# Performance work log

Measured on AMD Instinct MI355X. Metric: run time of the kernel, lower is better.

Reference implementation:

```python
import jax, jax.numpy as jnp
import numpy as np

N = 50000          # total nodes across the batched graphs
E = 800000         # edges (before self-loops)
D_IN = 128         # input_dim
D_H = 128          # hidden_channels
N_CLASSES = 2
N_GRAPHS = 64


def setup_inputs() -> dict:
    key = jax.random.key(0)
    ks = jax.random.split(key, 9)
    x = jax.random.normal(ks[0], (N, D_IN), dtype=jnp.float32)
    edge_index = jax.random.randint(ks[1], (2, E), 0, N, dtype=jnp.int64)
    batch = jnp.sort(jax.random.randint(ks[2], (N,), 0, N_GRAPHS, dtype=jnp.int64))
    s1 = 1.0 / np.sqrt(D_IN)
    s2 = 1.0 / np.sqrt(D_H)
    W1 = jax.random.uniform(ks[3], (D_IN, D_H), jnp.float32, -s1, s1)
    b1 = jnp.zeros((D_H,), jnp.float32)
    W2 = jax.random.uniform(ks[4], (D_H, D_H), jnp.float32, -s2, s2)
    b2 = jnp.zeros((D_H,), jnp.float32)
    Wfc = jax.random.uniform(ks[5], (D_H, N_CLASSES), jnp.float32, -s2, s2)
    bfc = jnp.zeros((N_CLASSES,), jnp.float32)
    return {"x": x, "edge_index": edge_index, "batch": batch,
            "W1": W1, "b1": b1, "W2": W2, "b2": b2, "Wfc": Wfc, "bfc": bfc}


def _gcn_conv(x, src, dst, norm, W, b):
    # GCNConv: h = W x, then out_i = sum_{j->i} norm_ij * h_j + b
    h = x @ W                                   # [N, D]
    msg = h[src] * norm[:, None]                # gather + scale, [E+N, D]
    out = jax.ops.segment_sum(msg, dst, num_segments=N)
    return out + b


def reference(x, edge_index, batch, W1, b1, W2, b2, Wfc, bfc):
    loops = jnp.arange(N, dtype=edge_index.dtype)
    src = jnp.concatenate([edge_index[0], loops])  # add self-loops
    dst = jnp.concatenate([edge_index[1], loops])
    # symmetric normalization D^-1/2 (A+I) D^-1/2
    deg = jax.ops.segment_sum(jnp.ones_like(dst, x.dtype), dst, num_segments=N)
    dinv = jax.lax.rsqrt(deg)                      # deg >= 1 due to self-loops
    norm = dinv[src] * dinv[dst]                   # [E+N]

    h = jax.nn.relu(_gcn_conv(x, src, dst, norm, W1, b1))
    h = _gcn_conv(h, src, dst, norm, W2, b2)

    # global_mean_pool over graph ids
    summed = jax.ops.segment_sum(h, batch, num_segments=N_GRAPHS)
    counts = jax.ops.segment_sum(jnp.ones((N,), x.dtype), batch, num_segments=N_GRAPHS)
    pooled = summed / jnp.maximum(counts, 1.0)[:, None]

    return pooled @ Wfc + bfc                      # [N_GRAPHS, N_CLASSES]
```

## Files before the change

### kernel.cpp

```cpp
#include <hip/hip_runtime.h>
#include <hip/hip_fp16.h>


#define N_NODES 50000
#define N_EDGES 800000
#define ETOT (N_EDGES + N_NODES)
#define D 128
#define NG 64
#define NC 2
#define JT 128
#define NBLK_W ((N_NODES + JT - 1) / JT)
#define NODES_PAD (NBLK_W * JT)
#define WT_F4 (NODES_PAD * NG / 4)
#define Q_F4 (NG * D / 4)

__global__ void k_init(int* __restrict__ deg, float4* __restrict__ wT4,
                       float4* __restrict__ q4, float* __restrict__ cnt,
                       int* __restrict__ cursor) {
    int i = blockIdx.x * 256 + threadIdx.x;
    float4 z = {0.f, 0.f, 0.f, 0.f};
    if (i < WT_F4) wT4[i] = z;
    if (i < Q_F4)  q4[i] = z;
    if (i < N_NODES) deg[i] = 1;
    if (i < NG)    cnt[i] = 0.f;
    if (i == 0)    *cursor = 0;
}

__global__ void k_deg(const int* __restrict__ ei, int* __restrict__ deg) {
    int e = blockIdx.x * 256 + threadIdx.x;
    if (e < N_EDGES) atomicAdd(&deg[ei[N_EDGES + e]], 1);
}

__global__ __launch_bounds__(256) void k_off(const int* __restrict__ deg,
                                             int* __restrict__ cursor,
                                             int* __restrict__ off,
                                             int* __restrict__ cur,
                                             float* __restrict__ dinv,
                                             const int* __restrict__ batch,
                                             float* __restrict__ cnt) {
    __shared__ int sh[256];
    __shared__ int base;
    __shared__ float scnt[NG];
    int t = threadIdx.x;
    int n = blockIdx.x * 256 + t;
    if (t < NG) scnt[t] = 0.f;
    int dg = (n < N_NODES) ? deg[n] : 0;
    sh[t] = dg;
    __syncthreads();
    for (int o = 1; o < 256; o <<= 1) {
        int u = (t >= o) ? sh[t - o] : 0;
        __syncthreads();
        sh[t] += u;
        __syncthreads();
    }
    if (t == 255) base = atomicAdd(cursor, sh[255]);
    __syncthreads();
    if (n < N_NODES) {
        int o2 = base + sh[t] - dg;
        off[n] = o2;
        cur[n] = o2;
        dinv[n] = rsqrtf((float)dg);
        atomicAdd(&scnt[batch[n]], 1.f);
    }
    __syncthreads();
    if (t < NG) {
        float v = scnt[t];
        if (v > 0.f) atomicAdd(&cnt[t], v);
    }
}

__global__ void k_scatter(const int* __restrict__ ei, int* __restrict__ cur,
                          const float* __restrict__ dinv,
                          const int* __restrict__ batch,
                          int* __restrict__ csr, float* __restrict__ csrw,
                          float* __restrict__ wT) {
    int e = blockIdx.x * 256 + threadIdx.x;
    if (e >= ETOT) return;
    int s, d2;
    if (e < N_EDGES) { s = ei[e]; d2 = ei[N_EDGES + e]; }
    else             { s = e - N_EDGES; d2 = s; }
    float nw = dinv[s] * dinv[d2];
    int p = atomicAdd(&cur[d2], 1);
    csr[p]  = s;
    csrw[p] = nw;
    atomicAdd(&wT[(size_t)s * NG + batch[d2]], nw);
}

__global__ __launch_bounds__(256) void k_gemm(const float* __restrict__ A,
                                              const float* __restrict__ W,
                                              __half* __restrict__ C) {
    __shared__ float As[128][68];
    int tid = threadIdx.x;
    int row0 = blockIdx.x * 64;
    {
        int r  = tid >> 2;
        int f4 = tid & 3;
        int ra = row0 + r; if (ra >= N_NODES) ra = N_NODES - 1;
        const float* arow = A + (size_t)ra * D;
#pragma unroll 1
        for (int i = 0; i < 8; i++) {
            int k0 = f4 * 4 + i * 16;
            float4 v = *(const float4*)(arow + k0);
            As[k0 + 0][r] = v.x;
            As[k0 + 1][r] = v.y;
            As[k0 + 2][r] = v.z;
            As[k0 + 3][r] = v.w;
        }
    }
    __syncthreads();

    int tx = tid & 15;
    int ty = tid >> 4;
    float acc[4][8];
#pragma unroll
    for (int i = 0; i < 4; i++)
#pragma unroll
        for (int j = 0; j < 8; j++) acc[i][j] = 0.f;

    const float* wp = W + tx * 8;
#pragma unroll 4
    for (int k = 0; k < 128; k++) {
        float4 a  = *(const float4*)&As[k][ty * 4];
        float4 b0 = *(const float4*)(wp + k * 128);
        float4 b1 = *(const float4*)(wp + k * 128 + 4);
        float av[4] = {a.x, a.y, a.z, a.w};
        float bv[8] = {b0.x, b0.y, b0.z, b0.w, b1.x, b1.y, b1.z, b1.w};
#pragma unroll
        for (int i = 0; i < 4; i++)
#pragma unroll
            for (int j = 0; j < 8; j++) acc[i][j] = fmaf(av[i], bv[j], acc[i][j]);
    }

#pragma unroll 1
    for (int i = 0; i < 4; i++) {
        int r = row0 + ty * 4 + i;
        if (r < N_NODES) {
            __half2 hh[4];
#pragma unroll
            for (int k2 = 0; k2 < 4; k2++)
                hh[k2] = __floats2half2_rn(acc[i][2 * k2], acc[i][2 * k2 + 1]);
            *(float4*)(C + (size_t)r * D + tx * 8) = *(float4*)hh;
        }
    }
}

__global__ __launch_bounds__(256) void k_agg(const __half* __restrict__ h,
                                             const int* __restrict__ off,
                                             const int* __restrict__ deg,
                                             const int* __restrict__ csr,
                                             const float* __restrict__ csrw,
                                             const float* __restrict__ bias,
                                             float* __restrict__ outp) {
    int n    = (blockIdx.x * 256 + threadIdx.x) >> 6;
    int lane = threadIdx.x & 63;
    if (n >= N_NODES) return;
    int beg = off[n], end = beg + deg[n];
    const __half2* hb = (const __half2*)h + lane;

    float ax = 0.f, ay = 0.f, bx = 0.f, by = 0.f;
    float cx = 0.f, cy = 0.f, dx = 0.f, dy = 0.f;
    int p = beg;
    for (; p + 8 <= end; p += 8) {
        int s0 = csr[p],     s1 = csr[p + 1], s2 = csr[p + 2], s3 = csr[p + 3];
        int s4 = csr[p + 4], s5 = csr[p + 5], s6 = csr[p + 6], s7 = csr[p + 7];
        float w0 = csrw[p],     w1 = csrw[p + 1], w2 = csrw[p + 2], w3 = csrw[p + 3];
        float w4 = csrw[p + 4], w5 = csrw[p + 5], w6 = csrw[p + 6], w7 = csrw[p + 7];
        float2 v0 = __half22float2(hb[(size_t)s0 * 64]);
        float2 v1 = __half22float2(hb[(size_t)s1 * 64]);
        float2 v2 = __half22float2(hb[(size_t)s2 * 64]);
        float2 v3 = __half22float2(hb[(size_t)s3 * 64]);
        float2 v4 = __half22float2(hb[(size_t)s4 * 64]);
        float2 v5 = __half22float2(hb[(size_t)s5 * 64]);
        float2 v6 = __half22float2(hb[(size_t)s6 * 64]);
        float2 v7 = __half22float2(hb[(size_t)s7 * 64]);
        ax = fmaf(w0, v0.x, ax); ay = fmaf(w0, v0.y, ay);
        bx = fmaf(w1, v1.x, bx); by = fmaf(w1, v1.y, by);
        cx = fmaf(w2, v2.x, cx); cy = fmaf(w2, v2.y, cy);
        dx = fmaf(w3, v3.x, dx); dy = fmaf(w3, v3.y, dy);
        ax = fmaf(w4, v4.x, ax); ay = fmaf(w4, v4.y, ay);
        bx = fmaf(w5, v5.x, bx); by = fmaf(w5, v5.y, by);
        cx = fmaf(w6, v6.x, cx); cy = fmaf(w6, v6.y, cy);
        dx = fmaf(w7, v7.x, dx); dy = fmaf(w7, v7.y, dy);
    }
    for (; p < end; p++) {
        int s = csr[p];
        float w = csrw[p];
        float2 v = __half22float2(hb[(size_t)s * 64]);
        ax = fmaf(w, v.x, ax); ay = fmaf(w, v.y, ay);
    }
    float ox = (ax + bx) + (cx + dx);
    float oy = (ay + by) + (cy + dy);

    ox = fmaxf(ox + bias[2 * lane], 0.f);
    oy = fmaxf(oy + bias[2 * lane + 1], 0.f);
    float2 o = {ox, oy};
    *(float2*)(outp + (size_t)n * D + 2 * lane) = o;
}

__global__ __launch_bounds__(256) void k_wgemm(const float* __restrict__ wT,
                                               const float* __restrict__ g,
                                               float* __restrict__ q) {
    __shared__ float ws[JT][NG];
    int t = threadIdx.x;
    int j0 = blockIdx.x * JT;
    {
        const float4* src = (const float4*)(wT + (size_t)j0 * NG);
        float4* dst = (float4*)ws;
        for (int i = t; i < JT * NG / 4; i += 256) dst[i] = src[i];
    }
    __syncthreads();
    int d  = t & 127;
    int bg = t >> 7;
    float acc[32];
#pragma unroll
    for (int i = 0; i < 32; i++) acc[i] = 0.f;
    int jlim = N_NODES - j0; if (jlim > JT) jlim = JT;
    for (int jj = 0; jj < jlim; jj++) {
        float gv = g[(size_t)(j0 + jj) * D + d];
        const float* wrow = &ws[jj][bg * 32];
#pragma unroll
        for (int i = 0; i < 32; i++)
            acc[i] = fmaf(wrow[i], gv, acc[i]);
    }
    float* qb = q + (size_t)(bg * 32) * D + d;
#pragma unroll
    for (int i = 0; i < 32; i++)
        atomicAdd(qb + (size_t)i * D, acc[i]);
}

__global__ void k_head(const float* __restrict__ q, const float* __restrict__ cnt,
                       const float* __restrict__ W2, const float* __restrict__ b2,
                       const float* __restrict__ Wfc, const float* __restrict__ bfc,
                       float* __restrict__ outp) {
    __shared__ float pooled[D];
    int b = blockIdx.x, t = threadIdx.x;
    float cn = cnt[b];
    float pv = 0.f;
    if (cn > 0.f) {
        float acc = 0.f;
        for (int k = 0; k < D; k++)
            acc = fmaf(q[b * D + k], W2[k * D + t], acc);
        pv = acc / cn + b2[t];
    }
    pooled[t] = pv;
    __syncthreads();
    if (t < NC) {
        float acc = bfc[t];
        for (int k = 0; k < D; k++)
            acc = fmaf(pooled[k], Wfc[k * NC + t], acc);
        outp[b * NC + t] = acc;
    }
}

extern "C" void kernel_launch(void* const* d_in, const int* in_sizes, int n_in,
                              void* d_out, int out_size, void* d_ws, size_t ws_size,
                              hipStream_t stream) {
    const float* x     = (const float*)d_in[0];
    const int*   ei    = (const int*)  d_in[1];
    const int*   batch = (const int*)  d_in[2];
    const float* W1    = (const float*)d_in[3];
    const float* b1    = (const float*)d_in[4];
    const float* W2    = (const float*)d_in[5];
    const float* b2    = (const float*)d_in[6];
    const float* Wfc   = (const float*)d_in[7];
    const float* bfc   = (const float*)d_in[8];
    float* out = (float*)d_out;

    char* w = (char*)d_ws;
    auto alloc = [&](size_t bytes) {
        char* p = w;
        w += (bytes + 255) & ~(size_t)255;
        return p;
    };
    int*    deg    = (int*)   alloc((size_t)N_NODES * 4);
    float*  dinv   = (float*) alloc((size_t)N_NODES * 4);
    int*    off    = (int*)   alloc((size_t)N_NODES * 4);
    int*    cur    = (int*)   alloc((size_t)N_NODES * 4);
    int*    csr    = (int*)   alloc((size_t)ETOT * 4);
    float*  csrw   = (float*) alloc((size_t)ETOT * 4);
    int*    cursor = (int*)   alloc(256);
    __half* hbuf   = (__half*)alloc((size_t)N_NODES * D * 2);
    float*  gbuf   = (float*) alloc((size_t)N_NODES * D * 4);
    float*  wT     = (float*) alloc((size_t)NODES_PAD * NG * 4);
    float*  q      = (float*) alloc((size_t)NG * D * 4);
    float*  cnt    = (float*) alloc((size_t)NG * 4);

    k_init<<<(WT_F4 + 255) / 256, 256, 0, stream>>>(deg, (float4*)wT, (float4*)q, cnt, cursor);
    k_deg<<<(N_EDGES + 255) / 256, 256, 0, stream>>>(ei, deg);
    k_off<<<(N_NODES + 255) / 256, 256, 0, stream>>>(deg, cursor, off, cur, dinv, batch, cnt);
    k_scatter<<<(ETOT + 255) / 256, 256, 0, stream>>>(ei, cur, dinv, batch, csr, csrw, wT);

    k_gemm<<<(N_NODES + 63) / 64, 256, 0, stream>>>(x, W1, hbuf);
    k_agg<<<(N_NODES * 64 + 255) / 256, 256, 0, stream>>>(hbuf, off, deg, csr, csrw, b1, gbuf);

    k_wgemm<<<NBLK_W, 256, 0, stream>>>(wT, gbuf, q);
    k_head<<<NG, 128, 0, stream>>>(q, cnt, W2, b2, Wfc, bfc, out);
}
```

Before: 277.0 us.

## Drop per-edge weight array; factor dinv[dst] out of aggregation and split scatter

The CSR build no longer stores a per-edge normalization weight. The aggregation kernel instead gathers dinv[src] per neighbor and multiplies the row sum by dinv[dst] once at the end. The weighted pooling accumulation into wT is moved out of the scatter kernel into a separate k_wacc kernel. This removes the csrw writes and reads and shortens the atomic-heavy scatter kernel. In exchange it adds random dinv gathers in the aggregation loop and an extra launch that re-reads the edge list.

```diff
diff --git a/kernel.cpp b/kernel.cpp
--- a/kernel.cpp
+++ b/kernel.cpp
@@ -70,20 +70,25 @@
 }
 
 __global__ void k_scatter(const int* __restrict__ ei, int* __restrict__ cur,
-                          const float* __restrict__ dinv,
-                          const int* __restrict__ batch,
-                          int* __restrict__ csr, float* __restrict__ csrw,
-                          float* __restrict__ wT) {
+                          int* __restrict__ csr) {
     int e = blockIdx.x * 256 + threadIdx.x;
     if (e >= ETOT) return;
     int s, d2;
     if (e < N_EDGES) { s = ei[e]; d2 = ei[N_EDGES + e]; }
     else             { s = e - N_EDGES; d2 = s; }
-    float nw = dinv[s] * dinv[d2];
-    int p = atomicAdd(&cur[d2], 1);
-    csr[p]  = s;
-    csrw[p] = nw;
-    atomicAdd(&wT[(size_t)s * NG + batch[d2]], nw);
+    csr[atomicAdd(&cur[d2], 1)] = s;
+}
+
+__global__ void k_wacc(const int* __restrict__ ei,
+                       const float* __restrict__ dinv,
+                       const int* __restrict__ batch,
+                       float* __restrict__ wT) {
+    int e = blockIdx.x * 256 + threadIdx.x;
+    if (e >= ETOT) return;
+    int s, d2;
+    if (e < N_EDGES) { s = ei[e]; d2 = ei[N_EDGES + e]; }
+    else             { s = e - N_EDGES; d2 = s; }
+    atomicAdd(&wT[(size_t)s * NG + batch[d2]], dinv[s] * dinv[d2]);
 }
 
 __global__ __launch_bounds__(256) void k_gemm(const float* __restrict__ A,
@@ -148,13 +153,14 @@
                                              const int* __restrict__ off,
                                              const int* __restrict__ deg,
                                              const int* __restrict__ csr,
-                                             const float* __restrict__ csrw,
+                                             const float* __restrict__ dinv,
                                              const float* __restrict__ bias,
                                              float* __restrict__ outp) {
     int n    = (blockIdx.x * 256 + threadIdx.x) >> 6;
     int lane = threadIdx.x & 63;
     if (n >= N_NODES) return;
     int beg = off[n], end = beg + deg[n];
+    float dn = dinv[n];
     const __half2* hb = (const __half2*)h + lane;
 
     float ax = 0.f, ay = 0.f, bx = 0.f, by = 0.f;
@@ -163,8 +169,8 @@
     for (; p + 8 <= end; p += 8) {
         int s0 = csr[p],     s1 = csr[p + 1], s2 = csr[p + 2], s3 = csr[p + 3];
         int s4 = csr[p + 4], s5 = csr[p + 5], s6 = csr[p + 6], s7 = csr[p + 7];
-        float w0 = csrw[p],     w1 = csrw[p + 1], w2 = csrw[p + 2], w3 = csrw[p + 3];
-        float w4 = csrw[p + 4], w5 = csrw[p + 5], w6 = csrw[p + 6], w7 = csrw[p + 7];
+        float w0 = dinv[s0], w1 = dinv[s1], w2 = dinv[s2], w3 = dinv[s3];
+        float w4 = dinv[s4], w5 = dinv[s5], w6 = dinv[s6], w7 = dinv[s7];
         float2 v0 = __half22float2(hb[(size_t)s0 * 64]);
         float2 v1 = __half22float2(hb[(size_t)s1 * 64]);
         float2 v2 = __half22float2(hb[(size_t)s2 * 64]);
@@ -184,12 +190,12 @@
     }
     for (; p < end; p++) {
         int s = csr[p];
-        float w = csrw[p];
+        float w = dinv[s];
         float2 v = __half22float2(hb[(size_t)s * 64]);
         ax = fmaf(w, v.x, ax); ay = fmaf(w, v.y, ay);
     }
-    float ox = (ax + bx) + (cx + dx);
-    float oy = (ay + by) + (cy + dy);
+    float ox = ((ax + bx) + (cx + dx)) * dn;
+    float oy = ((ay + by) + (cy + dy)) * dn;
 
     ox = fmaxf(ox + bias[2 * lane], 0.f);
     oy = fmaxf(oy + bias[2 * lane + 1], 0.f);
@@ -277,7 +283,6 @@
     int*    off    = (int*)   alloc((size_t)N_NODES * 4);
     int*    cur    = (int*)   alloc((size_t)N_NODES * 4);
     int*    csr    = (int*)   alloc((size_t)ETOT * 4);
-    float*  csrw   = (float*) alloc((size_t)ETOT * 4);
     int*    cursor = (int*)   alloc(256);
     __half* hbuf   = (__half*)alloc((size_t)N_NODES * D * 2);
     float*  gbuf   = (float*) alloc((size_t)N_NODES * D * 4);
@@ -288,10 +293,11 @@
     k_init<<<(WT_F4 + 255) / 256, 256, 0, stream>>>(deg, (float4*)wT, (float4*)q, cnt, cursor);
     k_deg<<<(N_EDGES + 255) / 256, 256, 0, stream>>>(ei, deg);
     k_off<<<(N_NODES + 255) / 256, 256, 0, stream>>>(deg, cursor, off, cur, dinv, batch, cnt);
-    k_scatter<<<(ETOT + 255) / 256, 256, 0, stream>>>(ei, cur, dinv, batch, csr, csrw, wT);
+    k_scatter<<<(ETOT + 255) / 256, 256, 0, stream>>>(ei, cur, csr);
+    k_wacc<<<(ETOT + 255) / 256, 256, 0, stream>>>(ei, dinv, batch, wT);
 
     k_gemm<<<(N_NODES + 63) / 64, 256, 0, stream>>>(x, W1, hbuf);
-    k_agg<<<(N_NODES * 64 + 255) / 256, 256, 0, stream>>>(hbuf, off, deg, csr, csrw, b1, gbuf);
+    k_agg<<<(N_NODES * 64 + 255) / 256, 256, 0, stream>>>(hbuf, off, deg, csr, dinv, b1, gbuf);
 
     k_wgemm<<<NBLK_W, 256, 0, stream>>>(wT, gbuf, q);
     k_head<<<NG, 128, 0, stream>>>(q, cnt, W2, b2, Wfc, bfc, out);
```

After: 293.5 us. 1.06x slower.
